# Performance work log

Measured on AMD Instinct MI355X. Metric: run time of the kernel, lower is better.

Reference implementation:

```python
import jax, jax.numpy as jnp
import numpy as np

NUM_HEADS = 8
KERNEL_SEARCH = 5  # local attention window
EPS = 1e-5


def _layernorm(x, g, b):
    m = jnp.mean(x, axis=-1, keepdims=True)
    v = jnp.var(x, axis=-1, keepdims=True)
    return (x - m) / jnp.sqrt(v + EPS) * g + b


def _unfold3(x):
    # x: [N, C, H, W] -> [N, C*9, H*W]; matches torch F.unfold(kernel=3, pad=1)
    # ordering: channel-major, kernel position (row-major) minor.
    N, C, H, W = x.shape
    xp = jnp.pad(x, ((0, 0), (0, 0), (1, 1), (1, 1)))
    pats = jnp.stack([xp[:, :, i:i + H, j:j + W] for i in range(3) for j in range(3)], axis=2)
    return pats.reshape(N, C * 9, H * W)


def _sai2token(x, w_mlp):
    # x: [b, c, a, h, w] -> tokens [h*w, b*a, spa_dim]
    b, c, a, h, w = x.shape
    x = x.transpose(0, 2, 1, 3, 4).reshape(b * a, c, h, w)
    tok = _unfold3(x).transpose(2, 0, 1)  # [hw, b*a, c*9]
    return jnp.einsum('lnk,ek->lne', tok, w_mlp)


def _local_mask(h, w, k):
    # additive mask [h*w, h*w]: 0 inside local kxk window, -inf outside
    kl, kr = k // 2, k - k // 2
    ii = jnp.arange(h)
    jj = jnp.arange(w)
    okh = (ii[None, :] >= ii[:, None] - kl) & (ii[None, :] < ii[:, None] + kr)  # [h,h]
    okw = (jj[None, :] >= jj[:, None] - kl) & (jj[None, :] < jj[:, None] + kr)  # [w,w]
    ok = okh[:, None, :, None] & okw[None, :, None, :]  # [h,w,h,w]
    ok = ok.reshape(h * w, h * w)
    return jnp.where(ok, 0.0, -jnp.inf).astype(jnp.float32)


def _attention(qk_in, v_in, in_proj_w, out_proj_w, bias):
    # qk_in/v_in: [L, B, E]; torch nn.MultiheadAttention, no biases, eval mode
    L, B, E = qk_in.shape
    Dh = E // NUM_HEADS
    Wq, Wk, Wv = in_proj_w[:E], in_proj_w[E:2 * E], in_proj_w[2 * E:]
    q = jnp.einsum('lbe,fe->lbf', qk_in, Wq).reshape(L, B, NUM_HEADS, Dh)
    k = jnp.einsum('lbe,fe->lbf', qk_in, Wk).reshape(L, B, NUM_HEADS, Dh)
    v = jnp.einsum('lbe,fe->lbf', v_in, Wv).reshape(L, B, NUM_HEADS, Dh)
    scale = 1.0 / np.sqrt(Dh).astype(np.float32)
    scores = jnp.einsum('lbhd,mbhd->bhlm', q, k) * scale + bias[None, None]
    attn = jax.nn.softmax(scores, axis=-1)
    out = jnp.einsum('bhlm,mbhd->lbhd', attn, v).reshape(L, B, E)
    return jnp.einsum('lbe,fe->lbf', out, out_proj_w)


def reference(buffer, spa_position, w_mlp, ln1_g, ln1_b, in_proj_w, out_proj_w,
              ln2_g, ln2_b, ff_w1, ff_w2, conv_w):
    b, c, a, h, w = buffer.shape
    bias = _local_mask(h, w, KERNEL_SEARCH)
    tok = _sai2token(buffer, w_mlp)          # [hw, b*a, E]
    pe = _sai2token(spa_position, w_mlp)
    x = _layernorm(tok + pe, ln1_g, ln1_b)
    tok = _attention(x, tok, in_proj_w, out_proj_w, bias) + tok
    # feed-forward (dropout is identity in eval)
    ff = _layernorm(tok, ln2_g, ln2_b)
    ff = jax.nn.relu(jnp.einsum('lbe,fe->lbf', ff, ff_w1))
    tok = jnp.einsum('lbf,ef->lbe', ff, ff_w2) + tok
    # Token2SAI: '(h w) (b a) e -> b e a h w' then 1x1x1 conv3d
    buf = tok.reshape(h, w, b, a, -1).transpose(2, 4, 3, 0, 1)  # [b, E, a, h, w]
    return jnp.einsum('oe,beahw->boahw', conv_w, buf)


def setup_inputs() -> dict:
    key = jax.random.key(0)
    ks = jax.random.split(key, 8)
    b, c, a, h, w = 1, 64, 25, 32, 32
    E = 2 * c
    s = 0.02
    return {
        'buffer': jax.random.normal(ks[0], (b, c, a, h, w), jnp.float32),
        'spa_position': jax.random.normal(ks[1], (b, c, a, h, w), jnp.float32),
        'w_mlp': jax.random.normal(ks[2], (E, c * 9), jnp.float32) * s,
        'ln1_g': jnp.ones((E,), jnp.float32),
        'ln1_b': jnp.zeros((E,), jnp.float32),
        'in_proj_w': jax.random.normal(ks[3], (3 * E, E), jnp.float32) * s,
        'out_proj_w': jax.random.normal(ks[4], (E, E), jnp.float32) * s,
        'ln2_g': jnp.ones((E,), jnp.float32),
        'ln2_b': jnp.zeros((E,), jnp.float32),
        'ff_w1': jax.random.normal(ks[5], (2 * E, E), jnp.float32) * s,
        'ff_w2': jax.random.normal(ks[6], (E, 2 * E), jnp.float32) * s,
        'conv_w': jax.random.normal(ks[7], (c, E), jnp.float32) * s,
    }
```

## Files before the change

### kernel.cpp

```cpp
#include <hip/hip_runtime.h>
#include <math.h>

#define Lh 32
#define Lw 32
#define LL 1024
#define BN 25
#define EE 128
#define CC 64
#define NHD 8
#define DH 16
#define FFD 256
#define MROWS 25600

typedef __attribute__((ext_vector_type(8))) short short8;
typedef __attribute__((ext_vector_type(4))) float f32x4;

__device__ inline ushort f2b(float x) {
    union { float f; unsigned u; } v; v.f = x;
    unsigned r = (v.u + 0x7fffu + ((v.u >> 16) & 1u)) >> 16;
    return (ushort)r;
}
__device__ inline float b2f(ushort u) {
    union { unsigned u; float f; } v; v.u = ((unsigned)u) << 16;
    return v.f;
}
__device__ inline void unpack8(uint4 p, float* dst) {
    unsigned vals[4] = { p.x, p.y, p.z, p.w };
#pragma unroll
    for (int i = 0; i < 4; i++) {
        union { unsigned u; float f; } lo, hi;
        lo.u = (vals[i] & 0xffffu) << 16;
        hi.u = vals[i] & 0xffff0000u;
        dst[2 * i] = lo.f; dst[2 * i + 1] = hi.f;
    }
}

#define OFF_W2  0
#define OFF_WQK 73728
#define OFF_WV  106496
#define OFF_WO  122880
#define OFF_W1  139264
#define OFF_W2F 172032
#define OFF_WC  204800
#define W_TOTAL 212992

__global__ __launch_bounds__(256) void k_prep_w(
    const float* __restrict__ w_mlp, const float* __restrict__ in_proj,
    const float* __restrict__ out_proj, const float* __restrict__ ff_w1,
    const float* __restrict__ ff_w2, const float* __restrict__ conv_w,
    ushort* __restrict__ Wb)
{
    int i = blockIdx.x * 256 + threadIdx.x;
    if (i >= W_TOTAL) return;
    if (i < 73728) {
        int e = i / 576, k = i - e * 576;
        int tap = k >> 6, ch = k & 63;
        Wb[OFF_W2 + i] = f2b(w_mlp[e * 576 + ch * 9 + tap]);
        return;
    }
    i -= 73728;
    if (i < 32768) { Wb[OFF_WQK + i] = f2b(in_proj[i]); return; }
    i -= 32768;
    if (i < 16384) { Wb[OFF_WV + i] = f2b(in_proj[32768 + i]); return; }
    i -= 16384;
    if (i < 16384) {
        int e = i >> 7, kpos = i & 127;
        int c = kpos >> 5, q = (kpos >> 3) & 3, ii = kpos & 7;
        int orig = (2 * c + (ii >> 2)) * 16 + q * 4 + (ii & 3);
        Wb[OFF_WO + i] = f2b(out_proj[e * 128 + orig]);
        return;
    }
    i -= 16384;
    if (i < 32768) { Wb[OFF_W1 + i] = f2b(ff_w1[i]); return; }
    i -= 32768;
    if (i < 32768) {
        int e = i >> 8, kpos = i & 255;
        int c = kpos >> 5, q = (kpos >> 3) & 3, ii = kpos & 7;
        int orig = (2 * c + (ii >> 2)) * 16 + q * 4 + (ii & 3);
        Wb[OFF_W2F + i] = f2b(ff_w2[e * 256 + orig]);
        return;
    }
    i -= 32768;
    {
        int o = i >> 7, kpos = i & 127;
        int c = kpos >> 5, q = (kpos >> 3) & 3, ii = kpos & 7;
        int orig = (2 * c + (ii >> 2)) * 16 + q * 4 + (ii & 3);
        Wb[OFF_WC + i] = f2b(conv_w[o * 128 + orig]);
    }
}

__global__ __launch_bounds__(256) void k_prep_in(
    const float* __restrict__ buf, const float* __restrict__ spa,
    ushort* __restrict__ T, ushort* __restrict__ S)
{
    const int n = blockIdx.x, y = blockIdx.y;
    __shared__ float t0[64][33];
    __shared__ float t1[64][33];
    const int t = threadIdx.x;
    {
        int ch = t >> 2, x8 = (t & 3) * 8;
        const float* p = buf + ((size_t)(ch * BN + n) * LL + y * Lw + x8);
        const float* q = spa + ((size_t)(ch * BN + n) * LL + y * Lw + x8);
        float4 a0 = ((const float4*)p)[0], a1 = ((const float4*)p)[1];
        float4 b0 = ((const float4*)q)[0], b1 = ((const float4*)q)[1];
        float* d0 = &t0[ch][x8];
        float* d1 = &t1[ch][x8];
        d0[0] = a0.x; d0[1] = a0.y; d0[2] = a0.z; d0[3] = a0.w;
        d0[4] = a1.x; d0[5] = a1.y; d0[6] = a1.z; d0[7] = a1.w;
        d1[0] = a0.x + b0.x; d1[1] = a0.y + b0.y; d1[2] = a0.z + b0.z; d1[3] = a0.w + b0.w;
        d1[4] = a1.x + b1.x; d1[5] = a1.y + b1.y; d1[6] = a1.z + b1.z; d1[7] = a1.w + b1.w;
    }
    __syncthreads();
    {
        int x = t >> 3, c8 = (t & 7) * 8;
        union { ushort u[8]; uint4 v; } o0, o1;
#pragma unroll
        for (int j = 0; j < 8; j++) { o0.u[j] = f2b(t0[c8 + j][x]); o1.u[j] = f2b(t1[c8 + j][x]); }
        size_t base = (((size_t)n * Lh + y) * Lw + x) * 64 + c8;
        *(uint4*)(T + base) = o0.v;
        *(uint4*)(S + base) = o1.v;
    }
}

__global__ __launch_bounds__(256) void k_tok_qkv(
    const ushort* __restrict__ T, const ushort* __restrict__ S,
    const ushort* __restrict__ W2, const ushort* __restrict__ WQK,
    const ushort* __restrict__ WV, const float* __restrict__ g1,
    const float* __restrict__ b1, ushort* __restrict__ TOKb,
    ushort* __restrict__ Qh, ushort* __restrict__ Kh, ushort* __restrict__ Vh)
{
    const int n = blockIdx.x, y = blockIdx.y;
    __shared__ ushort At[3 * 34 * 72];
    __shared__ ushort As_[3 * 34 * 72];
    __shared__ ushort Xs[32 * 136];
    __shared__ ushort Vs[32 * 136];
    __shared__ float2 red[32][4];
    const int t = threadIdx.x;
    const uint4 z = make_uint4(0, 0, 0, 0);

    {
        int x = t >> 3, c8 = (t & 7) * 8;
#pragma unroll
        for (int dy = 0; dy < 3; dy++) {
            int yy = y + dy - 1;
            uint4 va = z, vs = z;
            if (yy >= 0 && yy < Lh) {
                size_t gi = (((size_t)n * Lh + yy) * Lw + x) * 64 + c8;
                va = *(const uint4*)(T + gi);
                vs = *(const uint4*)(S + gi);
            }
            *(uint4*)(At + (dy * 34 + x + 1) * 72 + c8) = va;
            *(uint4*)(As_ + (dy * 34 + x + 1) * 72 + c8) = vs;
        }
        if (t < 48) {
            int dy = t / 16, rem = t % 16;
            int colp = (rem >> 3) * 33, c8p = (rem & 7) * 8;
            *(uint4*)(At + (dy * 34 + colp) * 72 + c8p) = z;
            *(uint4*)(As_ + (dy * 34 + colp) * 72 + c8p) = z;
        }
    }
    __syncthreads();

    const int w = t >> 6, lane = t & 63;
    const int col = lane & 15, quad = lane >> 4;
    f32x4 accT[2][2] = {}, accS[2][2] = {};

    for (int tap = 0; tap < 9; tap++) {
        int dy = tap / 3, dx = tap % 3;
#pragma unroll
        for (int cc = 0; cc < 2; cc++) {
            int kg = tap * 64 + cc * 32 + quad * 8;
            short8 b0 = *(const short8*)(W2 + (size_t)(w * 32 + col) * 576 + kg);
            short8 bq = *(const short8*)(W2 + (size_t)(w * 32 + 16 + col) * 576 + kg);
            int abase = (dy * 34 + col + dx) * 72 + cc * 32 + quad * 8;
            short8 aT0 = *(const short8*)(At + abase);
            short8 aT1 = *(const short8*)(At + abase + 16 * 72);
            short8 aS0 = *(const short8*)(As_ + abase);
            short8 aS1 = *(const short8*)(As_ + abase + 16 * 72);
            accT[0][0] = __builtin_amdgcn_mfma_f32_16x16x32_bf16(aT0, b0, accT[0][0], 0, 0, 0);
            accT[0][1] = __builtin_amdgcn_mfma_f32_16x16x32_bf16(aT0, bq, accT[0][1], 0, 0, 0);
            accT[1][0] = __builtin_amdgcn_mfma_f32_16x16x32_bf16(aT1, b0, accT[1][0], 0, 0, 0);
            accT[1][1] = __builtin_amdgcn_mfma_f32_16x16x32_bf16(aT1, bq, accT[1][1], 0, 0, 0);
            accS[0][0] = __builtin_amdgcn_mfma_f32_16x16x32_bf16(aS0, b0, accS[0][0], 0, 0, 0);
            accS[0][1] = __builtin_amdgcn_mfma_f32_16x16x32_bf16(aS0, bq, accS[0][1], 0, 0, 0);
            accS[1][0] = __builtin_amdgcn_mfma_f32_16x16x32_bf16(aS1, b0, accS[1][0], 0, 0, 0);
            accS[1][1] = __builtin_amdgcn_mfma_f32_16x16x32_bf16(aS1, bq, accS[1][1], 0, 0, 0);
        }
    }

#pragma unroll
    for (int mi = 0; mi < 2; mi++)
#pragma unroll
        for (int r = 0; r < 4; r++) {
            float a0 = accS[mi][0][r], a1 = accS[mi][1][r];
            float ss = a0 + a1, qq = a0 * a0 + a1 * a1;
#pragma unroll
            for (int m = 1; m < 16; m <<= 1) {
                ss += __shfl_xor(ss, m, 64);
                qq += __shfl_xor(qq, m, 64);
            }
            if (col == 0) red[mi * 16 + quad * 4 + r][w] = make_float2(ss, qq);
        }
    __syncthreads();

    const float ga = g1[w * 32 + col],      ba = b1[w * 32 + col];
    const float gb = g1[w * 32 + 16 + col], bb = b1[w * 32 + 16 + col];
#pragma unroll
    for (int mi = 0; mi < 2; mi++)
#pragma unroll
        for (int r = 0; r < 4; r++) {
            int x = mi * 16 + quad * 4 + r;
            float2 p0 = red[x][0], p1 = red[x][1], p2 = red[x][2], p3 = red[x][3];
            float mean = (p0.x + p1.x + p2.x + p3.x) * (1.f / 128.f);
            float var  = (p0.y + p1.y + p2.y + p3.y) * (1.f / 128.f) - mean * mean;
            float rstd = rsqrtf(var + 1e-5f);
            int e0 = w * 32 + col, e1 = w * 32 + 16 + col;
            Xs[x * 136 + e0] = f2b((accS[mi][0][r] - mean) * rstd * ga + ba);
            Xs[x * 136 + e1] = f2b((accS[mi][1][r] - mean) * rstd * gb + bb);
            Vs[x * 136 + e0] = f2b(accT[mi][0][r]);
            Vs[x * 136 + e1] = f2b(accT[mi][1][r]);
        }
    __syncthreads();

    short8 xb[2][4], xv[2][4];
#pragma unroll
    for (int j = 0; j < 2; j++)
#pragma unroll
        for (int kc = 0; kc < 4; kc++) {
            xb[j][kc] = *(const short8*)(Xs + (j * 16 + col) * 136 + kc * 32 + quad * 8);
            xv[j][kc] = *(const short8*)(Vs + (j * 16 + col) * 136 + kc * 32 + quad * 8);
        }
    f32x4 Q[2][2] = {}, K[2][2] = {}, V[2][2] = {};
#pragma unroll
    for (int hj = 0; hj < 2; hj++) {
        int h = 2 * w + hj;
#pragma unroll
        for (int kc = 0; kc < 4; kc++) {
            short8 aq = *(const short8*)(WQK + (size_t)(h * 16 + col) * 128 + kc * 32 + quad * 8);
            short8 ak = *(const short8*)(WQK + (size_t)(128 + h * 16 + col) * 128 + kc * 32 + quad * 8);
            short8 av = *(const short8*)(WV + (size_t)(h * 16 + col) * 128 + kc * 32 + quad * 8);
#pragma unroll
            for (int j = 0; j < 2; j++) {
                Q[hj][j] = __builtin_amdgcn_mfma_f32_16x16x32_bf16(aq, xb[j][kc], Q[hj][j], 0, 0, 0);
                K[hj][j] = __builtin_amdgcn_mfma_f32_16x16x32_bf16(ak, xb[j][kc], K[hj][j], 0, 0, 0);
                V[hj][j] = __builtin_amdgcn_mfma_f32_16x16x32_bf16(av, xv[j][kc], V[hj][j], 0, 0, 0);
            }
        }
    }
#pragma unroll
    for (int hj = 0; hj < 2; hj++)
#pragma unroll
        for (int j = 0; j < 2; j++) {
            int h = 2 * w + hj;
            int l = y * 32 + j * 16 + col;
            size_t base = ((size_t)(n * 8 + h) * 1024 + l) * 16 + quad * 4;
            ushort4 oq, ok, ov;
            oq.x = f2b(Q[hj][j][0]); oq.y = f2b(Q[hj][j][1]); oq.z = f2b(Q[hj][j][2]); oq.w = f2b(Q[hj][j][3]);
            ok.x = f2b(K[hj][j][0]); ok.y = f2b(K[hj][j][1]); ok.z = f2b(K[hj][j][2]); ok.w = f2b(K[hj][j][3]);
            ov.x = f2b(V[hj][j][0]); ov.y = f2b(V[hj][j][1]); ov.z = f2b(V[hj][j][2]); ov.w = f2b(V[hj][j][3]);
            *(ushort4*)(Qh + base) = oq;
            *(ushort4*)(Kh + base) = ok;
            *(ushort4*)(Vh + base) = ov;
        }
#pragma unroll
    for (int k = 0; k < 2; k++) {
        int idx = t + k * 256;
        int r = idx >> 4, seg = idx & 15;
        *(uint4*)(TOKb + ((size_t)((y * 32 + r) * 25 + n)) * 128 + seg * 8) =
            *(const uint4*)(Vs + r * 136 + seg * 8);
    }
}

__global__ __launch_bounds__(256) void k_attn_oln(
    const ushort* __restrict__ Qh, const ushort* __restrict__ Kh,
    const ushort* __restrict__ Vh, const ushort* __restrict__ WOP,
    const float* __restrict__ g2, const float* __restrict__ b2,
    ushort* __restrict__ TOKb, ushort* __restrict__ XLN2)
{
    __shared__ ushort VT[4][16 * 168];
    __shared__ ushort OX[32 * 136];
    __shared__ ushort Rs[32 * 136];
    __shared__ float2 red[32][4];
    const int y = blockIdx.x, n = blockIdx.y;
    const int t = threadIdx.x, w = t >> 6, lane = t & 63;
    const int col = lane & 15, quad = lane >> 4;

    {
        int r = t >> 3, seg = t & 7;
        const uint4* src = (const uint4*)(TOKb + ((size_t)((y * 32 + r) * 25 + n)) * 128 + seg * 16);
        *(uint4*)(Rs + r * 136 + seg * 16)     = src[0];
        *(uint4*)(Rs + r * 136 + seg * 16 + 8) = src[1];
    }

    short8 z8 = {0, 0, 0, 0, 0, 0, 0, 0};
    f32x4 O2[2][2] = {};
#pragma unroll
    for (int hj = 0; hj < 2; hj++) {
        const int h = 2 * w + hj;
        const size_t base = (size_t)(n * 8 + h) * 1024;
        for (int i = lane; i < 160; i += 64) {
            int kr = i >> 5, kx = i & 31;
            int yyc = min(max(y - 2 + kr, 0), 31);
            const ushort* src = Vh + (base + yyc * 32 + kx) * 16;
            union { uint4 v; ushort u[8]; } ua, ub;
            ua.v = *(const uint4*)(src);
            ub.v = *(const uint4*)(src + 8);
            int pos = (kr << 5) + (((kx & 15) >> 2) << 3) + ((kx >> 4) << 2) + (kx & 3);
            ushort* dst = &VT[w][pos];
#pragma unroll
            for (int d = 0; d < 8; d++) dst[d * 168] = ua.u[d];
#pragma unroll
            for (int d = 0; d < 8; d++) dst[(d + 8) * 168] = ub.u[d];
        }

        short8 qf[2] = { z8, z8 };
#pragma unroll
        for (int j = 0; j < 2; j++)
            if (quad < 2)
                qf[j] = *(const short8*)(Qh + (base + y * 32 + j * 16 + col) * 16 + quad * 8);

        f32x4 Sc[2][10] = {};
#pragma unroll
        for (int tt = 0; tt < 10; tt++) {
            int kr = tt >> 1, kx = ((tt & 1) << 4) + col;
            int yyc = min(max(y - 2 + kr, 0), 31);
            short8 kf = z8;
            if (quad < 2)
                kf = *(const short8*)(Kh + (base + yyc * 32 + kx) * 16 + quad * 8);
            Sc[0][tt] = __builtin_amdgcn_mfma_f32_16x16x32_bf16(kf, qf[0], Sc[0][tt], 0, 0, 0);
            Sc[1][tt] = __builtin_amdgcn_mfma_f32_16x16x32_bf16(kf, qf[1], Sc[1][tt], 0, 0, 0);
        }

        float invs[2];
#pragma unroll
        for (int j = 0; j < 2; j++) {
            int qx = j * 16 + col;
            float mx = -1e30f;
#pragma unroll
            for (int tt = 0; tt < 10; tt++) {
                int yy = y - 2 + (tt >> 1);
                bool rok = (yy >= 0) && (yy < 32);
                int kxb = ((tt & 1) << 4) + quad * 4;
#pragma unroll
                for (int r = 0; r < 4; r++) {
                    int dd = kxb + r - qx;
                    bool ok = rok && ((unsigned)(dd + 2) <= 4u);
                    float v = ok ? Sc[j][tt][r] * 0.25f : -1e30f;
                    Sc[j][tt][r] = v;
                    mx = fmaxf(mx, v);
                }
            }
            mx = fmaxf(mx, __shfl_xor(mx, 16, 64));
            mx = fmaxf(mx, __shfl_xor(mx, 32, 64));
            float sum = 0.f;
#pragma unroll
            for (int tt = 0; tt < 10; tt++)
#pragma unroll
                for (int r = 0; r < 4; r++) {
                    float p = __expf(Sc[j][tt][r] - mx);
                    Sc[j][tt][r] = p;
                    sum += p;
                }
            sum += __shfl_xor(sum, 16, 64);
            sum += __shfl_xor(sum, 32, 64);
            invs[j] = 1.f / sum;
        }

#pragma unroll
        for (int c = 0; c < 5; c++) {
            short8 vt = *(const short8*)(&VT[w][col * 168 + c * 32 + quad * 8]);
#pragma unroll
            for (int j = 0; j < 2; j++) {
                union { ushort u[8]; short8 s; } pb;
#pragma unroll
                for (int i = 0; i < 8; i++)
                    pb.u[i] = f2b(Sc[j][2 * c + (i >> 2)][i & 3] * invs[j]);
                O2[hj][j] = __builtin_amdgcn_mfma_f32_16x16x32_bf16(vt, pb.s, O2[hj][j], 0, 0, 0);
            }
        }
    }

#pragma unroll
    for (int j = 0; j < 2; j++) {
        union { ushort u[8]; uint4 v; } pb;
#pragma unroll
        for (int i = 0; i < 8; i++)
            pb.u[i] = f2b(O2[i >> 2][j][i & 3]);
        *(uint4*)(OX + (j * 16 + col) * 136 + w * 32 + quad * 8) = pb.v;
    }
    __syncthreads();

    f32x4 Y[2][2] = {};
#pragma unroll
    for (int kc = 0; kc < 4; kc++) {
        short8 hb0 = *(const short8*)(OX + col * 136 + kc * 32 + quad * 8);
        short8 hb1 = *(const short8*)(OX + (16 + col) * 136 + kc * 32 + quad * 8);
#pragma unroll
        for (int jj = 0; jj < 2; jj++) {
            int et = 2 * w + jj;
            short8 a = *(const short8*)(WOP + (size_t)(et * 16 + col) * 128 + kc * 32 + quad * 8);
            Y[jj][0] = __builtin_amdgcn_mfma_f32_16x16x32_bf16(a, hb0, Y[jj][0], 0, 0, 0);
            Y[jj][1] = __builtin_amdgcn_mfma_f32_16x16x32_bf16(a, hb1, Y[jj][1], 0, 0, 0);
        }
    }
    float sum[2] = {0.f, 0.f}, sq[2] = {0.f, 0.f};
#pragma unroll
    for (int j = 0; j < 2; j++)
#pragma unroll
        for (int jj = 0; jj < 2; jj++)
#pragma unroll
            for (int r = 0; r < 4; r++) {
                int e = (2 * w + jj) * 16 + quad * 4 + r;
                float v = Y[jj][j][r] + b2f(Rs[(j * 16 + col) * 136 + e]);
                Y[jj][j][r] = v;
                sum[j] += v; sq[j] += v * v;
            }
#pragma unroll
    for (int j = 0; j < 2; j++) {
        sum[j] += __shfl_xor(sum[j], 16, 64); sum[j] += __shfl_xor(sum[j], 32, 64);
        sq[j]  += __shfl_xor(sq[j], 16, 64);  sq[j]  += __shfl_xor(sq[j], 32, 64);
        if (quad == 0) red[j * 16 + col][w] = make_float2(sum[j], sq[j]);
    }
    __syncthreads();

    float mean[2], rstd[2];
#pragma unroll
    for (int j = 0; j < 2; j++) {
        float2 p0 = red[j * 16 + col][0], p1 = red[j * 16 + col][1];
        float2 p2 = red[j * 16 + col][2], p3 = red[j * 16 + col][3];
        mean[j] = (p0.x + p1.x + p2.x + p3.x) * (1.f / 128.f);
        float var = (p0.y + p1.y + p2.y + p3.y) * (1.f / 128.f) - mean[j] * mean[j];
        rstd[j] = rsqrtf(var + 1e-5f);
    }
#pragma unroll
    for (int jj = 0; jj < 2; jj++)
#pragma unroll
        for (int r = 0; r < 4; r++) {
            int e = (2 * w + jj) * 16 + quad * 4 + r;
            float ge = g2[e], be = b2[e];
#pragma unroll
            for (int j = 0; j < 2; j++) {
                float v = Y[jj][j][r];
                Rs[(j * 16 + col) * 136 + e] = f2b(v);
                OX[(j * 16 + col) * 136 + e] = f2b((v - mean[j]) * rstd[j] * ge + be);
            }
        }
    __syncthreads();

    {
        int r = t >> 3, seg = t & 7;
        size_t go = ((size_t)((y * 32 + r) * 25 + n)) * 128 + seg * 16;
        *(uint4*)(TOKb + go)     = *(const uint4*)(Rs + r * 136 + seg * 16);
        *(uint4*)(TOKb + go + 8) = *(const uint4*)(Rs + r * 136 + seg * 16 + 8);
        *(uint4*)(XLN2 + go)     = *(const uint4*)(OX + r * 136 + seg * 16);
        *(uint4*)(XLN2 + go + 8) = *(const uint4*)(OX + r * 136 + seg * 16 + 8);
    }
}

__global__ __launch_bounds__(256) void k_ffn(
    const ushort* __restrict__ XLN2, const ushort* __restrict__ TOKb,
    const ushort* __restrict__ W1, const ushort* __restrict__ W2P,
    const ushort* __restrict__ WCP, float* __restrict__ out)
{
    __shared__ ushort Xs[16 * 136];
    __shared__ float  Rsp[16 * 132];
    __shared__ ushort Hs[16 * 264];
    __shared__ ushort Ys[16 * 136];
    const int b = blockIdx.x, bn = b % 25, l0 = (b / 25) * 16;
    const int t = threadIdx.x, w = t >> 6, lane = t & 63;
    const int col = lane & 15, quad = lane >> 4;

    {
        int r = t >> 4, seg = t & 15;
        size_t m = (size_t)(l0 + r) * 25 + bn;
        *(uint4*)(Xs + r * 136 + seg * 8) = *(const uint4*)(XLN2 + m * 128 + seg * 8);
        uint4 tb = *(const uint4*)(TOKb + m * 128 + seg * 8);
        float fv[8];
        unpack8(tb, fv);
#pragma unroll
        for (int j = 0; j < 8; j++) {
            int e = seg * 8 + j;
            int c = e >> 5, half = (e >> 4) & 1, q = (e >> 2) & 3, r2 = e & 3;
            Rsp[r * 132 + c * 32 + q * 8 + half * 4 + r2] = fv[j];
        }
    }
    __syncthreads();

    short8 xb[4];
#pragma unroll
    for (int kc = 0; kc < 4; kc++)
        xb[kc] = *(const short8*)(Xs + col * 136 + kc * 32 + quad * 8);

    f32x4 H[4] = {};
#pragma unroll
    for (int j = 0; j < 4; j++) {
        int ft = 4 * w + j;
#pragma unroll
        for (int kc = 0; kc < 4; kc++) {
            short8 a = *(const short8*)(W1 + (size_t)(ft * 16 + col) * 128 + kc * 32 + quad * 8);
            H[j] = __builtin_amdgcn_mfma_f32_16x16x32_bf16(a, xb[kc], H[j], 0, 0, 0);
        }
    }
#pragma unroll
    for (int cc = 0; cc < 2; cc++) {
        union { ushort u[8]; uint4 v; } pb;
#pragma unroll
        for (int i = 0; i < 8; i++)
            pb.u[i] = f2b(fmaxf(H[2 * cc + (i >> 2)][i & 3], 0.f));
        *(uint4*)(Hs + col * 264 + (2 * w + cc) * 32 + quad * 8) = pb.v;
    }
    __syncthreads();

    f32x4 Y[2] = {};
#pragma unroll
    for (int kc = 0; kc < 8; kc++) {
        short8 hb = *(const short8*)(Hs + col * 264 + kc * 32 + quad * 8);
#pragma unroll
        for (int j = 0; j < 2; j++) {
            int et = 2 * w + j;
            short8 a = *(const short8*)(W2P + (size_t)(et * 16 + col) * 256 + kc * 32 + quad * 8);
            Y[j] = __builtin_amdgcn_mfma_f32_16x16x32_bf16(a, hb, Y[j], 0, 0, 0);
        }
    }
    {
        float4 r0 = *(const float4*)(Rsp + col * 132 + w * 32 + quad * 8);
        float4 r1 = *(const float4*)(Rsp + col * 132 + w * 32 + quad * 8 + 4);
        union { ushort u[8]; uint4 v; } pb;
        pb.u[0] = f2b(Y[0][0] + r0.x); pb.u[1] = f2b(Y[0][1] + r0.y);
        pb.u[2] = f2b(Y[0][2] + r0.z); pb.u[3] = f2b(Y[0][3] + r0.w);
        pb.u[4] = f2b(Y[1][0] + r1.x); pb.u[5] = f2b(Y[1][1] + r1.y);
        pb.u[6] = f2b(Y[1][2] + r1.z); pb.u[7] = f2b(Y[1][3] + r1.w);
        *(uint4*)(Ys + col * 136 + w * 32 + quad * 8) = pb.v;
    }
    __syncthreads();

    f32x4 O = {};
#pragma unroll
    for (int c = 0; c < 4; c++) {
        short8 yb = *(const short8*)(Ys + col * 136 + c * 32 + quad * 8);
        short8 a = *(const short8*)(WCP + (size_t)(w * 16 + col) * 128 + c * 32 + quad * 8);
        O = __builtin_amdgcn_mfma_f32_16x16x32_bf16(a, yb, O, 0, 0, 0);
    }
    const int l = l0 + col;
#pragma unroll
    for (int r2 = 0; r2 < 4; r2++) {
        int o = w * 16 + quad * 4 + r2;
        out[(size_t)(o * 25 + bn) * 1024 + l] = O[r2];
    }
}

extern "C" void kernel_launch(void* const* d_in, const int* in_sizes, int n_in,
                              void* d_out, int out_size, void* d_ws, size_t ws_size,
                              hipStream_t stream)
{
    const float* buffer   = (const float*)d_in[0];
    const float* spa      = (const float*)d_in[1];
    const float* w_mlp    = (const float*)d_in[2];
    const float* ln1_g    = (const float*)d_in[3];
    const float* ln1_b    = (const float*)d_in[4];
    const float* in_proj  = (const float*)d_in[5];
    const float* out_proj = (const float*)d_in[6];
    const float* ln2_g    = (const float*)d_in[7];
    const float* ln2_b    = (const float*)d_in[8];
    const float* ff_w1    = (const float*)d_in[9];
    const float* ff_w2    = (const float*)d_in[10];
    const float* conv_w   = (const float*)d_in[11];
    float* out = (float*)d_out;

    char* ws = (char*)d_ws;
    ushort* TOKb = (ushort*)(ws);
    ushort* XLN2 = (ushort*)(ws + 6553600);
    ushort* Qh   = (ushort*)(ws + 13107200);
    ushort* Kh   = (ushort*)(ws + 19660800);
    ushort* Vh   = (ushort*)(ws + 26214400);
    ushort* Tbf  = (ushort*)(ws + 32768000);
    ushort* Sbf  = (ushort*)(ws + 36044800);
    ushort* Wb   = (ushort*)(ws + 39321600);

    k_prep_w<<<dim3((W_TOTAL + 255) / 256), 256, 0, stream>>>(
        w_mlp, in_proj, out_proj, ff_w1, ff_w2, conv_w, Wb);
    k_prep_in<<<dim3(BN, Lh), 256, 0, stream>>>(buffer, spa, Tbf, Sbf);
    k_tok_qkv<<<dim3(BN, Lh), 256, 0, stream>>>(Tbf, Sbf, Wb + OFF_W2,
                                                Wb + OFF_WQK, Wb + OFF_WV,
                                                ln1_g, ln1_b, TOKb, Qh, Kh, Vh);
    k_attn_oln<<<dim3(Lh, BN), 256, 0, stream>>>(Qh, Kh, Vh, Wb + OFF_WO,
                                                 ln2_g, ln2_b, TOKb, XLN2);
    k_ffn<<<dim3(1600), 256, 0, stream>>>(XLN2, TOKb, Wb + OFF_W1, Wb + OFF_W2F,
                                          Wb + OFF_WC, out);
}
```

Measured before the change: 191.8 us.

## Store V pre-transposed in global memory and split attention blocks by half-row

The QKV kernel now writes V straight into a transposed, MFMA-ready global layout, so the attention kernel no longer stages and transposes V through shared memory. The attention kernel handles 16 query columns per block instead of 32, doubling the grid to 1600 blocks and halving register and shared-memory use per block. Both kernels also remap block indices so that adjacent blocks are spread across 8 groups, likely aimed at XCD locality. In exchange, V is written with scattered 2-byte global stores, and each K/V row is read by two blocks instead of one.

After: 183.3 us. -4.4%, faster.

```diff
diff --git a/kernel.cpp b/kernel.cpp
--- a/kernel.cpp
+++ b/kernel.cpp
@@ -127,9 +127,11 @@
     const ushort* __restrict__ W2, const ushort* __restrict__ WQK,
     const ushort* __restrict__ WV, const float* __restrict__ g1,
     const float* __restrict__ b1, ushort* __restrict__ TOKb,
-    ushort* __restrict__ Qh, ushort* __restrict__ Kh, ushort* __restrict__ Vh)
+    ushort* __restrict__ Qh, ushort* __restrict__ Kh, ushort* __restrict__ VTg)
 {
-    const int n = blockIdx.x, y = blockIdx.y;
+    const int bid = blockIdx.x;
+    const int idx = (bid & 7) * 100 + (bid >> 3);
+    const int n = idx / 32, y = idx & 31;
     __shared__ ushort At[3 * 34 * 72];
     __shared__ ushort As_[3 * 34 * 72];
     __shared__ ushort Xs[32 * 136];
@@ -248,24 +250,28 @@
         }
     }
 #pragma unroll
-    for (int hj = 0; hj < 2; hj++)
+    for (int hj = 0; hj < 2; hj++) {
+        int h = 2 * w + hj;
+        size_t vrow = ((size_t)(n * 8 + h) * 32 + y) * 512;
 #pragma unroll
         for (int j = 0; j < 2; j++) {
-            int h = 2 * w + hj;
             int l = y * 32 + j * 16 + col;
             size_t base = ((size_t)(n * 8 + h) * 1024 + l) * 16 + quad * 4;
-            ushort4 oq, ok, ov;
+            ushort4 oq, ok;
             oq.x = f2b(Q[hj][j][0]); oq.y = f2b(Q[hj][j][1]); oq.z = f2b(Q[hj][j][2]); oq.w = f2b(Q[hj][j][3]);
             ok.x = f2b(K[hj][j][0]); ok.y = f2b(K[hj][j][1]); ok.z = f2b(K[hj][j][2]); ok.w = f2b(K[hj][j][3]);
-            ov.x = f2b(V[hj][j][0]); ov.y = f2b(V[hj][j][1]); ov.z = f2b(V[hj][j][2]); ov.w = f2b(V[hj][j][3]);
             *(ushort4*)(Qh + base) = oq;
             *(ushort4*)(Kh + base) = ok;
-            *(ushort4*)(Vh + base) = ov;
-        }
+            int xp = ((col >> 2) << 3) + (j << 2) + (col & 3);
+#pragma unroll
+            for (int r = 0; r < 4; r++)
+                VTg[vrow + (quad * 4 + r) * 32 + xp] = f2b(V[hj][j][r]);
+        }
+    }
 #pragma unroll
     for (int k = 0; k < 2; k++) {
-        int idx = t + k * 256;
-        int r = idx >> 4, seg = idx & 15;
+        int idx2 = t + k * 256;
+        int r = idx2 >> 4, seg = idx2 & 15;
         *(uint4*)(TOKb + ((size_t)((y * 32 + r) * 25 + n)) * 128 + seg * 8) =
             *(const uint4*)(Vs + r * 136 + seg * 8);
     }
@@ -273,53 +279,40 @@
 
 __global__ __launch_bounds__(256) void k_attn_oln(
     const ushort* __restrict__ Qh, const ushort* __restrict__ Kh,
-    const ushort* __restrict__ Vh, const ushort* __restrict__ WOP,
+    const ushort* __restrict__ VTg, const ushort* __restrict__ WOP,
     const float* __restrict__ g2, const float* __restrict__ b2,
     ushort* __restrict__ TOKb, ushort* __restrict__ XLN2)
 {
-    __shared__ ushort VT[4][16 * 168];
-    __shared__ ushort OX[32 * 136];
-    __shared__ ushort Rs[32 * 136];
-    __shared__ float2 red[32][4];
-    const int y = blockIdx.x, n = blockIdx.y;
+    __shared__ ushort OX[16 * 136];
+    __shared__ ushort Rs[16 * 136];
+    __shared__ float2 red[16][4];
+    const int bid = blockIdx.x;
+    const int idx = (bid & 7) * 200 + (bid >> 3);
+    const int n = idx / 64, rem = idx & 63;
+    const int y = rem >> 1, half = rem & 1;
     const int t = threadIdx.x, w = t >> 6, lane = t & 63;
     const int col = lane & 15, quad = lane >> 4;
 
     {
-        int r = t >> 3, seg = t & 7;
-        const uint4* src = (const uint4*)(TOKb + ((size_t)((y * 32 + r) * 25 + n)) * 128 + seg * 16);
-        *(uint4*)(Rs + r * 136 + seg * 16)     = src[0];
-        *(uint4*)(Rs + r * 136 + seg * 16 + 8) = src[1];
+        int r = t >> 4, seg = t & 15;
+        *(uint4*)(Rs + r * 136 + seg * 8) =
+            *(const uint4*)(TOKb + ((size_t)((y * 32 + half * 16 + r) * 25 + n)) * 128 + seg * 8);
     }
 
     short8 z8 = {0, 0, 0, 0, 0, 0, 0, 0};
-    f32x4 O2[2][2] = {};
+    const int qx = half * 16 + col;
+    f32x4 O2[2] = {};
 #pragma unroll
     for (int hj = 0; hj < 2; hj++) {
         const int h = 2 * w + hj;
         const size_t base = (size_t)(n * 8 + h) * 1024;
-        for (int i = lane; i < 160; i += 64) {
-            int kr = i >> 5, kx = i & 31;
-            int yyc = min(max(y - 2 + kr, 0), 31);
-            const ushort* src = Vh + (base + yyc * 32 + kx) * 16;
-            union { uint4 v; ushort u[8]; } ua, ub;
-            ua.v = *(const uint4*)(src);
-            ub.v = *(const uint4*)(src + 8);
-            int pos = (kr << 5) + (((kx & 15) >> 2) << 3) + ((kx >> 4) << 2) + (kx & 3);
-            ushort* dst = &VT[w][pos];
-#pragma unroll
-            for (int d = 0; d < 8; d++) dst[d * 168] = ua.u[d];
-#pragma unroll
-            for (int d = 0; d < 8; d++) dst[(d + 8) * 168] = ub.u[d];
-        }
-
-        short8 qf[2] = { z8, z8 };
-#pragma unroll
-        for (int j = 0; j < 2; j++)
-            if (quad < 2)
-                qf[j] = *(const short8*)(Qh + (base + y * 32 + j * 16 + col) * 16 + quad * 8);
-
-        f32x4 Sc[2][10] = {};
+        const size_t vbase = ((size_t)(n * 8 + h) * 32) * 512;
+
+        short8 qf = z8;
+        if (quad < 2)
+            qf = *(const short8*)(Qh + (base + y * 32 + half * 16 + col) * 16 + quad * 8);
+
+        f32x4 Sc[10] = {};
 #pragma unroll
         for (int tt = 0; tt < 10; tt++) {
             int kr = tt >> 1, kx = ((tt & 1) << 4) + col;
@@ -327,133 +320,106 @@
             short8 kf = z8;
             if (quad < 2)
                 kf = *(const short8*)(Kh + (base + yyc * 32 + kx) * 16 + quad * 8);
-            Sc[0][tt] = __builtin_amdgcn_mfma_f32_16x16x32_bf16(kf, qf[0], Sc[0][tt], 0, 0, 0);
-            Sc[1][tt] = __builtin_amdgcn_mfma_f32_16x16x32_bf16(kf, qf[1], Sc[1][tt], 0, 0, 0);
-        }
-
-        float invs[2];
-#pragma unroll
-        for (int j = 0; j < 2; j++) {
-            int qx = j * 16 + col;
-            float mx = -1e30f;
-#pragma unroll
-            for (int tt = 0; tt < 10; tt++) {
-                int yy = y - 2 + (tt >> 1);
-                bool rok = (yy >= 0) && (yy < 32);
-                int kxb = ((tt & 1) << 4) + quad * 4;
-#pragma unroll
-                for (int r = 0; r < 4; r++) {
-                    int dd = kxb + r - qx;
-                    bool ok = rok && ((unsigned)(dd + 2) <= 4u);
-                    float v = ok ? Sc[j][tt][r] * 0.25f : -1e30f;
-                    Sc[j][tt][r] = v;
-                    mx = fmaxf(mx, v);
-                }
+            Sc[tt] = __builtin_amdgcn_mfma_f32_16x16x32_bf16(kf, qf, Sc[tt], 0, 0, 0);
+        }
+
+        float mx = -1e30f;
+#pragma unroll
+        for (int tt = 0; tt < 10; tt++) {
+            int yy = y - 2 + (tt >> 1);
+            bool rok = (yy >= 0) && (yy < 32);
+            int kxb = ((tt & 1) << 4) + quad * 4;
+#pragma unroll
+            for (int r = 0; r < 4; r++) {
+                int dd = kxb + r - qx;
+                bool ok = rok && ((unsigned)(dd + 2) <= 4u);
+                float v = ok ? Sc[tt][r] * 0.25f : -1e30f;
+                Sc[tt][r] = v;
+                mx = fmaxf(mx, v);
             }
-            mx = fmaxf(mx, __shfl_xor(mx, 16, 64));
-            mx = fmaxf(mx, __shfl_xor(mx, 32, 64));
-            float sum = 0.f;
-#pragma unroll
-            for (int tt = 0; tt < 10; tt++)
-#pragma unroll
-                for (int r = 0; r < 4; r++) {
-                    float p = __expf(Sc[j][tt][r] - mx);
-                    Sc[j][tt][r] = p;
-                    sum += p;
-                }
-            sum += __shfl_xor(sum, 16, 64);
-            sum += __shfl_xor(sum, 32, 64);
-            invs[j] = 1.f / sum;
-        }
+        }
+        mx = fmaxf(mx, __shfl_xor(mx, 16, 64));
+        mx = fmaxf(mx, __shfl_xor(mx, 32, 64));
+        float sum = 0.f;
+#pragma unroll
+        for (int tt = 0; tt < 10; tt++)
+#pragma unroll
+            for (int r = 0; r < 4; r++) {
+                float p = __expf(Sc[tt][r] - mx);
+                Sc[tt][r] = p;
+                sum += p;
+            }
+        sum += __shfl_xor(sum, 16, 64);
+        sum += __shfl_xor(sum, 32, 64);
+        const float inv = 1.f / sum;
 
 #pragma unroll
         for (int c = 0; c < 5; c++) {
-            short8 vt = *(const short8*)(&VT[w][col * 168 + c * 32 + quad * 8]);
-#pragma unroll
-            for (int j = 0; j < 2; j++) {
-                union { ushort u[8]; short8 s; } pb;
-#pragma unroll
-                for (int i = 0; i < 8; i++)
-                    pb.u[i] = f2b(Sc[j][2 * c + (i >> 2)][i & 3] * invs[j]);
-                O2[hj][j] = __builtin_amdgcn_mfma_f32_16x16x32_bf16(vt, pb.s, O2[hj][j], 0, 0, 0);
-            }
-        }
-    }
-
-#pragma unroll
-    for (int j = 0; j < 2; j++) {
+            int yyc = min(max(y - 2 + c, 0), 31);
+            short8 vt = *(const short8*)(VTg + vbase + (size_t)yyc * 512 + col * 32 + quad * 8);
+            union { ushort u[8]; short8 s; } pb;
+#pragma unroll
+            for (int i = 0; i < 8; i++)
+                pb.u[i] = f2b(Sc[2 * c + (i >> 2)][i & 3] * inv);
+            O2[hj] = __builtin_amdgcn_mfma_f32_16x16x32_bf16(vt, pb.s, O2[hj], 0, 0, 0);
+        }
+    }
+
+    {
         union { ushort u[8]; uint4 v; } pb;
 #pragma unroll
         for (int i = 0; i < 8; i++)
-            pb.u[i] = f2b(O2[i >> 2][j][i & 3]);
-        *(uint4*)(OX + (j * 16 + col) * 136 + w * 32 + quad * 8) = pb.v;
-    }
-    __syncthreads();
-
-    f32x4 Y[2][2] = {};
+            pb.u[i] = f2b(O2[i >> 2][i & 3]);
+        *(uint4*)(OX + col * 136 + w * 32 + quad * 8) = pb.v;
+    }
+    __syncthreads();
+
+    f32x4 Y[2] = {};
 #pragma unroll
     for (int kc = 0; kc < 4; kc++) {
-        short8 hb0 = *(const short8*)(OX + col * 136 + kc * 32 + quad * 8);
-        short8 hb1 = *(const short8*)(OX + (16 + col) * 136 + kc * 32 + quad * 8);
+        short8 hb = *(const short8*)(OX + col * 136 + kc * 32 + quad * 8);
 #pragma unroll
         for (int jj = 0; jj < 2; jj++) {
             int et = 2 * w + jj;
             short8 a = *(const short8*)(WOP + (size_t)(et * 16 + col) * 128 + kc * 32 + quad * 8);
-            Y[jj][0] = __builtin_amdgcn_mfma_f32_16x16x32_bf16(a, hb0, Y[jj][0], 0, 0, 0);
-            Y[jj][1] = __builtin_amdgcn_mfma_f32_16x16x32_bf16(a, hb1, Y[jj][1], 0, 0, 0);
-        }
-    }
-    float sum[2] = {0.f, 0.f}, sq[2] = {0.f, 0.f};
-#pragma unroll
-    for (int j = 0; j < 2; j++)
-#pragma unroll
-        for (int jj = 0; jj < 2; jj++)
-#pragma unroll
-            for (int r = 0; r < 4; r++) {
-                int e = (2 * w + jj) * 16 + quad * 4 + r;
-                float v = Y[jj][j][r] + b2f(Rs[(j * 16 + col) * 136 + e]);
-                Y[jj][j][r] = v;
-                sum[j] += v; sq[j] += v * v;
-            }
-#pragma unroll
-    for (int j = 0; j < 2; j++) {
-        sum[j] += __shfl_xor(sum[j], 16, 64); sum[j] += __shfl_xor(sum[j], 32, 64);
-        sq[j]  += __shfl_xor(sq[j], 16, 64);  sq[j]  += __shfl_xor(sq[j], 32, 64);
-        if (quad == 0) red[j * 16 + col][w] = make_float2(sum[j], sq[j]);
-    }
-    __syncthreads();
-
-    float mean[2], rstd[2];
-#pragma unroll
-    for (int j = 0; j < 2; j++) {
-        float2 p0 = red[j * 16 + col][0], p1 = red[j * 16 + col][1];
-        float2 p2 = red[j * 16 + col][2], p3 = red[j * 16 + col][3];
-        mean[j] = (p0.x + p1.x + p2.x + p3.x) * (1.f / 128.f);
-        float var = (p0.y + p1.y + p2.y + p3.y) * (1.f / 128.f) - mean[j] * mean[j];
-        rstd[j] = rsqrtf(var + 1e-5f);
-    }
+            Y[jj] = __builtin_amdgcn_mfma_f32_16x16x32_bf16(a, hb, Y[jj], 0, 0, 0);
+        }
+    }
+    float sum = 0.f, sq = 0.f;
 #pragma unroll
     for (int jj = 0; jj < 2; jj++)
 #pragma unroll
         for (int r = 0; r < 4; r++) {
             int e = (2 * w + jj) * 16 + quad * 4 + r;
-            float ge = g2[e], be = b2[e];
-#pragma unroll
-            for (int j = 0; j < 2; j++) {
-                float v = Y[jj][j][r];
-                Rs[(j * 16 + col) * 136 + e] = f2b(v);
-                OX[(j * 16 + col) * 136 + e] = f2b((v - mean[j]) * rstd[j] * ge + be);
-            }
-        }
-    __syncthreads();
-
-    {
-        int r = t >> 3, seg = t & 7;
-        size_t go = ((size_t)((y * 32 + r) * 25 + n)) * 128 + seg * 16;
-        *(uint4*)(TOKb + go)     = *(const uint4*)(Rs + r * 136 + seg * 16);
-        *(uint4*)(TOKb + go + 8) = *(const uint4*)(Rs + r * 136 + seg * 16 + 8);
-        *(uint4*)(XLN2 + go)     = *(const uint4*)(OX + r * 136 + seg * 16);
-        *(uint4*)(XLN2 + go + 8) = *(const uint4*)(OX + r * 136 + seg * 16 + 8);
+            float v = Y[jj][r] + b2f(Rs[col * 136 + e]);
+            Y[jj][r] = v;
+            sum += v; sq += v * v;
+        }
+    sum += __shfl_xor(sum, 16, 64); sum += __shfl_xor(sum, 32, 64);
+    sq  += __shfl_xor(sq, 16, 64);  sq  += __shfl_xor(sq, 32, 64);
+    if (quad == 0) red[col][w] = make_float2(sum, sq);
+    __syncthreads();
+
+    float2 p0 = red[col][0], p1 = red[col][1], p2 = red[col][2], p3 = red[col][3];
+    float mean = (p0.x + p1.x + p2.x + p3.x) * (1.f / 128.f);
+    float var  = (p0.y + p1.y + p2.y + p3.y) * (1.f / 128.f) - mean * mean;
+    float rstd = rsqrtf(var + 1e-5f);
+#pragma unroll
+    for (int jj = 0; jj < 2; jj++)
+#pragma unroll
+        for (int r = 0; r < 4; r++) {
+            int e = (2 * w + jj) * 16 + quad * 4 + r;
+            float v = Y[jj][r];
+            Rs[col * 136 + e] = f2b(v);
+            OX[col * 136 + e] = f2b((v - mean) * rstd * g2[e] + b2[e]);
+        }
+    __syncthreads();
+
+    {
+        int r = t >> 4, seg = t & 15;
+        size_t go = ((size_t)((y * 32 + half * 16 + r) * 25 + n)) * 128 + seg * 8;
+        *(uint4*)(TOKb + go) = *(const uint4*)(Rs + r * 136 + seg * 8);
+        *(uint4*)(XLN2 + go) = *(const uint4*)(OX + r * 136 + seg * 8);
     }
 }
 
@@ -480,8 +446,8 @@
 #pragma unroll
         for (int j = 0; j < 8; j++) {
             int e = seg * 8 + j;
-            int c = e >> 5, half = (e >> 4) & 1, q = (e >> 2) & 3, r2 = e & 3;
-            Rsp[r * 132 + c * 32 + q * 8 + half * 4 + r2] = fv[j];
+            int c = e >> 5, halfb = (e >> 4) & 1, q = (e >> 2) & 3, r2 = e & 3;
+            Rsp[r * 132 + c * 32 + q * 8 + halfb * 4 + r2] = fv[j];
         }
     }
     __syncthreads();
@@ -572,7 +538,7 @@
     ushort* XLN2 = (ushort*)(ws + 6553600);
     ushort* Qh   = (ushort*)(ws + 13107200);
     ushort* Kh   = (ushort*)(ws + 19660800);
-    ushort* Vh   = (ushort*)(ws + 26214400);
+    ushort* VTg  = (ushort*)(ws + 26214400);
     ushort* Tbf  = (ushort*)(ws + 32768000);
     ushort* Sbf  = (ushort*)(ws + 36044800);
     ushort* Wb   = (ushort*)(ws + 39321600);
@@ -580,11 +546,11 @@
     k_prep_w<<<dim3((W_TOTAL + 255) / 256), 256, 0, stream>>>(
         w_mlp, in_proj, out_proj, ff_w1, ff_w2, conv_w, Wb);
     k_prep_in<<<dim3(BN, Lh), 256, 0, stream>>>(buffer, spa, Tbf, Sbf);
-    k_tok_qkv<<<dim3(BN, Lh), 256, 0, stream>>>(Tbf, Sbf, Wb + OFF_W2,
-                                                Wb + OFF_WQK, Wb + OFF_WV,
-                                                ln1_g, ln1_b, TOKb, Qh, Kh, Vh);
-    k_attn_oln<<<dim3(Lh, BN), 256, 0, stream>>>(Qh, Kh, Vh, Wb + OFF_WO,
-                                                 ln2_g, ln2_b, TOKb, XLN2);
+    k_tok_qkv<<<dim3(800), 256, 0, stream>>>(Tbf, Sbf, Wb + OFF_W2,
+                                             Wb + OFF_WQK, Wb + OFF_WV,
+                                             ln1_g, ln1_b, TOKb, Qh, Kh, VTg);
+    k_attn_oln<<<dim3(1600), 256, 0, stream>>>(Qh, Kh, VTg, Wb + OFF_WO,
+                                               ln2_g, ln2_b, TOKb, XLN2);
     k_ffn<<<dim3(1600), 256, 0, stream>>>(XLN2, TOKb, Wb + OFF_W1, Wb + OFF_W2F,
                                           Wb + OFF_WC, out);
 }
```
